# Kernel tuning notes

Hardware: AMD Instinct MI355X
Metric: run time of the kernel (lower is better)

The kernel has to match this reference:

```python
import jax, jax.numpy as jnp
import numpy as np

B, S = 4096, 256
D = 32  # output_size // 4


def setup_inputs() -> dict:
    key = jax.random.key(0)
    ks = jax.random.split(key, 32)
    # continuous features
    cont_p = jax.random.normal(ks[0], (B, S, 3), dtype=jnp.float32)
    cont_c = jax.random.normal(ks[1], (B, S, 2), dtype=jnp.float32)
    # categorical features, per-column vocab sizes from Embedding tables
    vocabs_p = [2, 2, 2, 11, 34]
    cat_p = jnp.stack([
        jax.random.randint(ks[2 + i], (B, S), 0, v, dtype=jnp.int32)
        for i, v in enumerate(vocabs_p)], axis=2)
    vocabs_c = [19, 31]
    cat_c = jnp.stack([
        jax.random.randint(ks[7 + i], (B, S), 0, v, dtype=jnp.int32)
        for i, v in enumerate(vocabs_c)], axis=2)
    lengths = jax.random.randint(ks[9], (B,), 1, S + 1, dtype=jnp.int32)

    def lin(k, fan_in, fan_out):
        bound = 1.0 / np.sqrt(fan_in)
        kw, kb = jax.random.split(k)
        w = jax.random.uniform(kw, (fan_in, fan_out), jnp.float32, -bound, bound)
        b = jax.random.uniform(kb, (fan_out,), jnp.float32, -bound, bound)
        return w, b

    w_p1, b_p1 = lin(ks[10], 3, D)
    w_p2, b_p2 = lin(ks[11], D, D)
    w_c1, b_c1 = lin(ks[12], 2, D)
    w_c2, b_c2 = lin(ks[13], D, D)
    emb_gender = jax.random.normal(ks[14], (2, D), dtype=jnp.float32)
    emb_korean = jax.random.normal(ks[15], (2, D), dtype=jnp.float32)
    emb_primary = jax.random.normal(ks[16], (2, D), dtype=jnp.float32)
    emb_job = jax.random.normal(ks[17], (11, D), dtype=jnp.float32)
    emb_rep = jax.random.normal(ks[18], (34, D), dtype=jnp.float32)
    emb_place = jax.random.normal(ks[19], (19, D), dtype=jnp.float32)
    emb_add = jax.random.normal(ks[20], (31, D), dtype=jnp.float32)
    w_fc1, b_fc1 = lin(ks[21], 128, 64)
    w_fc2, b_fc2 = lin(ks[22], 64, 2)

    return dict(cont_p=cont_p, cont_c=cont_c, cat_p=cat_p, cat_c=cat_c,
                lengths=lengths,
                w_p1=w_p1, b_p1=b_p1, w_p2=w_p2, b_p2=b_p2,
                w_c1=w_c1, b_c1=b_c1, w_c2=w_c2, b_c2=b_c2,
                emb_gender=emb_gender, emb_korean=emb_korean,
                emb_primary=emb_primary, emb_job=emb_job, emb_rep=emb_rep,
                emb_place=emb_place, emb_add=emb_add,
                w_fc1=w_fc1, b_fc1=b_fc1, w_fc2=w_fc2, b_fc2=b_fc2)


def reference(cont_p, cont_c, cat_p, cat_c, lengths,
              w_p1, b_p1, w_p2, b_p2, w_c1, b_c1, w_c2, b_c2,
              emb_gender, emb_korean, emb_primary, emb_job, emb_rep,
              emb_place, emb_add, w_fc1, b_fc1, w_fc2, b_fc2):
    # small per-token MLPs on continuous features -> [B,S,D]
    hp = jax.nn.relu(cont_p @ w_p1 + b_p1) @ w_p2 + b_p2
    hc = jax.nn.relu(cont_c @ w_c1 + b_c1) @ w_c2 + b_c2
    # multi-table embedding lookups, averaged per group -> [B,S,D]
    ep = (emb_gender[cat_p[:, :, 0]] + emb_korean[cat_p[:, :, 1]] +
          emb_primary[cat_p[:, :, 2]] + emb_job[cat_p[:, :, 3]] +
          emb_rep[cat_p[:, :, 4]]) / 5.0
    ec = (emb_place[cat_c[:, :, 0]] + emb_add[cat_c[:, :, 1]]) / 2.0
    # concat order matches torch: (cat_p, cat_c, cont_p, cont_c) -> [B,S,128]
    x = jnp.concatenate([ep, ec, hp, hc], axis=2)
    # ragged mean pool over first lengths[i] positions (masked segment mean)
    mask = (jnp.arange(x.shape[1])[None, :] < lengths[:, None])
    pooled = jnp.sum(x * mask[:, :, None], axis=1) / lengths[:, None].astype(x.dtype)
    # head: relu(fc1) -> relu(fc2); dropout p=0.0 is identity
    h = jax.nn.relu(pooled @ w_fc1 + b_fc1)
    return jax.nn.relu(h @ w_fc2 + b_fc2)
```

## Files before the change

kernel.cpp:

```cpp
#include <hip/hip_runtime.h>


#define BDIM 64

__global__ __launch_bounds__(BDIM)
void mlpreg_kernel(const float* __restrict__ cont_p,
                   const float* __restrict__ cont_c,
                   const int* __restrict__ cat_p,
                   const int* __restrict__ cat_c,
                   const int* __restrict__ lengths,
                   const float* __restrict__ w_p1, const float* __restrict__ b_p1,
                   const float* __restrict__ w_p2, const float* __restrict__ b_p2,
                   const float* __restrict__ w_c1, const float* __restrict__ b_c1,
                   const float* __restrict__ w_c2, const float* __restrict__ b_c2,
                   const float* __restrict__ emb_g,  const float* __restrict__ emb_k,
                   const float* __restrict__ emb_pr, const float* __restrict__ emb_j,
                   const float* __restrict__ emb_r,  const float* __restrict__ emb_pl,
                   const float* __restrict__ emb_a,
                   const float* __restrict__ w_fc1, const float* __restrict__ b_fc1,
                   const float* __restrict__ w_fc2, const float* __restrict__ b_fc2,
                   float* __restrict__ out)
{
    constexpr int S = 256;
    __shared__ float sP[2][S * 3];
    __shared__ float sC[2][S * 2];
    __shared__ int   hist[2][96];
    __shared__ float sPacc[2][64];
    __shared__ float sPool[2][128];

    const int lane = threadIdx.x;
    const int b0 = blockIdx.x * 2, b1 = b0 + 1;

    int L0 = lengths[b0]; L0 = (L0 < 1) ? 1 : (L0 > S ? S : L0);
    int L1 = lengths[b1]; L1 = (L1 < 1) ? 1 : (L1 > S ? S : L1);
    const float L0f = (float)L0, L1f = (float)L1;
    const float invL0 = 1.0f / L0f, invL1 = 1.0f / L1f;

    { int i = lane;            ((int*)hist)[i] = 0;
      i += 64;                 ((int*)hist)[i] = 0;
      i += 64;                 ((int*)hist)[i] = 0; }

    const int ch = lane & 31, h = lane >> 5;
    const float wp0 = w_p1[ch], wp1 = w_p1[32 + ch], wp2 = w_p1[64 + ch], bp = b_p1[ch];
    const float wc0 = w_c1[ch], wc1 = w_c1[32 + ch], bc = b_c1[ch];

    {
        const float4* gp0 = (const float4*)(cont_p + (size_t)b0 * (S * 3));
        const float4* gp1 = (const float4*)(cont_p + (size_t)b1 * (S * 3));
        const float4* gc0 = (const float4*)(cont_c + (size_t)b0 * (S * 2));
        const float4* gc1 = (const float4*)(cont_c + (size_t)b1 * (S * 2));
        const int n0 = (3 * L0 + 3) >> 2, n1 = (3 * L1 + 3) >> 2;
        const int m0 = (2 * L0 + 3) >> 2, m1 = (2 * L1 + 3) >> 2;
        for (int i = lane; i < n0; i += 64) *(float4*)&sP[0][4 * i] = gp0[i];
        for (int i = lane; i < n1; i += 64) *(float4*)&sP[1][4 * i] = gp1[i];
        for (int i = lane; i < m0; i += 64) *(float4*)&sC[0][4 * i] = gc0[i];
        for (int i = lane; i < m1; i += 64) *(float4*)&sC[1][4 * i] = gc1[i];
    }

    int sg0 = 0, sk0 = 0, sp0 = 0, sg1 = 0, sk1 = 0, sp1 = 0;
    {
        const int*  kp0 = cat_p + (size_t)b0 * (S * 5);
        const int*  kp1 = cat_p + (size_t)b1 * (S * 5);
        const int2* kc0 = (const int2*)(cat_c + (size_t)b0 * (S * 2));
        const int2* kc1 = (const int2*)(cat_c + (size_t)b1 * (S * 2));
        #pragma unroll 2
        for (int t = lane; t < L0; t += 64) {
            int v0 = kp0[5 * t], v1 = kp0[5 * t + 1], v2 = kp0[5 * t + 2],
                v3 = kp0[5 * t + 3], v4 = kp0[5 * t + 4];
            int2 q = kc0[t];
            sg0 += v0; sk0 += v1; sp0 += v2;
            atomicAdd(&hist[0][v3], 1);
            atomicAdd(&hist[0][11 + v4], 1);
            atomicAdd(&hist[0][45 + q.x], 1);
            atomicAdd(&hist[0][64 + q.y], 1);
        }
        #pragma unroll 2
        for (int t = lane; t < L1; t += 64) {
            int v0 = kp1[5 * t], v1 = kp1[5 * t + 1], v2 = kp1[5 * t + 2],
                v3 = kp1[5 * t + 3], v4 = kp1[5 * t + 4];
            int2 q = kc1[t];
            sg1 += v0; sk1 += v1; sp1 += v2;
            atomicAdd(&hist[1][v3], 1);
            atomicAdd(&hist[1][11 + v4], 1);
            atomicAdd(&hist[1][45 + q.x], 1);
            atomicAdd(&hist[1][64 + q.y], 1);
        }
    }
    #pragma unroll
    for (int d = 32; d; d >>= 1) {
        sg0 += __shfl_xor(sg0, d); sk0 += __shfl_xor(sk0, d); sp0 += __shfl_xor(sp0, d);
        sg1 += __shfl_xor(sg1, d); sk1 += __shfl_xor(sk1, d); sp1 += __shfl_xor(sp1, d);
    }
    __syncthreads();

    {
        const int   Lr   = h ? L1 : L0;
        const float invr = h ? invL1 : invL0;
        const float* tp = sP[h];
        const float* tc = sC[h];
        float aP = 0.f, aC = 0.f;
        #pragma unroll 4
        for (int t = 0; t < Lr; ++t) {
            float c0 = tp[3 * t], c1 = tp[3 * t + 1], c2 = tp[3 * t + 2];
            float2 d2 = *(const float2*)&tc[2 * t];
            aP += fmaxf(fmaf(c0, wp0, fmaf(c1, wp1, fmaf(c2, wp2, bp))), 0.f);
            aC += fmaxf(fmaf(d2.x, wc0, fmaf(d2.y, wc1, bc)), 0.f);
        }
        sPacc[h][ch]      = aP * invr;
        sPacc[h][32 + ch] = aC * invr;
    }
    __syncthreads();

    if (h == 0) {
        float g0 = emb_g[ch],  g1 = emb_g[32 + ch];
        float k0 = emb_k[ch],  k1 = emb_k[32 + ch];
        float p0 = emb_pr[ch], p1 = emb_pr[32 + ch];
        float fg0 = (float)sg0, fk0 = (float)sk0, fp0 = (float)sp0;
        float fg1 = (float)sg1, fk1 = (float)sk1, fp1 = (float)sp1;
        float A0 = fmaf(L0f - fg0, g0, fg0 * g1) + fmaf(L0f - fk0, k0, fk0 * k1)
                 + fmaf(L0f - fp0, p0, fp0 * p1);
        float A1 = fmaf(L1f - fg1, g0, fg1 * g1) + fmaf(L1f - fk1, k0, fk1 * k1)
                 + fmaf(L1f - fp1, p0, fp1 * p1);
        #pragma unroll
        for (int r = 0; r < 11; ++r) {
            float w = emb_j[r * 32 + ch];
            A0 = fmaf((float)hist[0][r], w, A0);
            A1 = fmaf((float)hist[1][r], w, A1);
        }
        #pragma unroll
        for (int r = 0; r < 34; ++r) {
            float w = emb_r[r * 32 + ch];
            A0 = fmaf((float)hist[0][11 + r], w, A0);
            A1 = fmaf((float)hist[1][11 + r], w, A1);
        }
        sPool[0][ch] = A0 * (invL0 * 0.2f);
        sPool[1][ch] = A1 * (invL1 * 0.2f);

        float v0 = b_p2[ch], v1 = v0;
        #pragma unroll
        for (int k = 0; k < 32; ++k) {
            float w = w_p2[k * 32 + ch];
            v0 = fmaf(sPacc[0][k], w, v0);
            v1 = fmaf(sPacc[1][k], w, v1);
        }
        sPool[0][64 + ch] = v0;
        sPool[1][64 + ch] = v1;
    } else {
        float A0 = 0.f, A1 = 0.f;
        #pragma unroll
        for (int r = 0; r < 19; ++r) {
            float w = emb_pl[r * 32 + ch];
            A0 = fmaf((float)hist[0][45 + r], w, A0);
            A1 = fmaf((float)hist[1][45 + r], w, A1);
        }
        #pragma unroll
        for (int r = 0; r < 31; ++r) {
            float w = emb_a[r * 32 + ch];
            A0 = fmaf((float)hist[0][64 + r], w, A0);
            A1 = fmaf((float)hist[1][64 + r], w, A1);
        }
        sPool[0][32 + ch] = A0 * (invL0 * 0.5f);
        sPool[1][32 + ch] = A1 * (invL1 * 0.5f);

        float v0 = b_c2[ch], v1 = v0;
        #pragma unroll
        for (int k = 0; k < 32; ++k) {
            float w = w_c2[k * 32 + ch];
            v0 = fmaf(sPacc[0][32 + k], w, v0);
            v1 = fmaf(sPacc[1][32 + k], w, v1);
        }
        sPool[0][96 + ch] = v0;
        sPool[1][96 + ch] = v1;
    }
    __syncthreads();

    {
        const int o = lane;
        float x0 = b_fc1[o], y0 = 0.f;
        float x1 = x0,       y1 = 0.f;
        #pragma unroll 8
        for (int k = 0; k < 128; k += 2) {
            float wa = w_fc1[(size_t)k * 64 + o];
            float wb = w_fc1[(size_t)(k + 1) * 64 + o];
            float u0 = sPool[0][k], u1 = sPool[0][k + 1];
            float s0 = sPool[1][k], s1 = sPool[1][k + 1];
            x0 = fmaf(u0, wa, x0); y0 = fmaf(u1, wb, y0);
            x1 = fmaf(s0, wa, x1); y1 = fmaf(s1, wb, y1);
        }
        float h0 = fmaxf(x0 + y0, 0.f);
        float h1 = fmaxf(x1 + y1, 0.f);
        float wa = w_fc2[2 * o], wb = w_fc2[2 * o + 1];
        float q00 = h0 * wa, q01 = h0 * wb, q10 = h1 * wa, q11 = h1 * wb;
        #pragma unroll
        for (int d = 32; d; d >>= 1) {
            q00 += __shfl_xor(q00, d); q01 += __shfl_xor(q01, d);
            q10 += __shfl_xor(q10, d); q11 += __shfl_xor(q11, d);
        }
        if (lane == 0) {
            float bb0 = b_fc2[0], bb1 = b_fc2[1];
            float4 o4;
            o4.x = fmaxf(q00 + bb0, 0.f);
            o4.y = fmaxf(q01 + bb1, 0.f);
            o4.z = fmaxf(q10 + bb0, 0.f);
            o4.w = fmaxf(q11 + bb1, 0.f);
            *(float4*)&out[(size_t)b0 * 2] = o4;
        }
    }
}

extern "C" void kernel_launch(void* const* d_in, const int* in_sizes, int n_in,
                              void* d_out, int out_size, void* d_ws, size_t ws_size,
                              hipStream_t stream) {
    const float* cont_p = (const float*)d_in[0];
    const float* cont_c = (const float*)d_in[1];
    const int*   cat_p  = (const int*)d_in[2];
    const int*   cat_c  = (const int*)d_in[3];
    const int*   lens   = (const int*)d_in[4];
    const float* w_p1   = (const float*)d_in[5];
    const float* b_p1   = (const float*)d_in[6];
    const float* w_p2   = (const float*)d_in[7];
    const float* b_p2   = (const float*)d_in[8];
    const float* w_c1   = (const float*)d_in[9];
    const float* b_c1   = (const float*)d_in[10];
    const float* w_c2   = (const float*)d_in[11];
    const float* b_c2   = (const float*)d_in[12];
    const float* emb_g  = (const float*)d_in[13];
    const float* emb_k  = (const float*)d_in[14];
    const float* emb_pr = (const float*)d_in[15];
    const float* emb_j  = (const float*)d_in[16];
    const float* emb_r  = (const float*)d_in[17];
    const float* emb_pl = (const float*)d_in[18];
    const float* emb_a  = (const float*)d_in[19];
    const float* w_fc1  = (const float*)d_in[20];
    const float* b_fc1  = (const float*)d_in[21];
    const float* w_fc2  = (const float*)d_in[22];
    const float* b_fc2  = (const float*)d_in[23];
    float* out = (float*)d_out;

    hipLaunchKernelGGL(mlpreg_kernel, dim3(2048), dim3(BDIM), 0, stream,
                       cont_p, cont_c, cat_p, cat_c, lens,
                       w_p1, b_p1, w_p2, b_p2, w_c1, b_c1, w_c2, b_c2,
                       emb_g, emb_k, emb_pr, emb_j, emb_r, emb_pl, emb_a,
                       w_fc1, b_fc1, w_fc2, b_fc2, out);
}
```

Baseline: 139.9 us.

## Interleave token features in shared memory, pack categorical sums, vectorize fc1

Continuous features for each token are now staged into one interleaved shared array with a stride of 8, so the per-token MLP loop reads a float4 plus a scalar instead of five scattered loads. The three binary categorical sums are packed into a single int with 10-bit fields, cutting the warp shuffle reductions from six values to two. The histogram loop is unrolled into four fixed 64-token blocks, and the fc1 loop reads pooled vectors as float4. The staging loop now does scalar loads with a divide by 3 instead of float4 copies, which adds integer work and non-vector global loads.

```diff
diff --git a/kernel.cpp b/kernel.cpp
--- a/kernel.cpp
+++ b/kernel.cpp
@@ -2,6 +2,7 @@
 
 
 #define BDIM 64
+#define S 256
 
 __global__ __launch_bounds__(BDIM)
 void mlpreg_kernel(const float* __restrict__ cont_p,
@@ -21,93 +22,92 @@
                    const float* __restrict__ w_fc2, const float* __restrict__ b_fc2,
                    float* __restrict__ out)
 {
-    constexpr int S = 256;
-    __shared__ float sP[2][S * 3];
-    __shared__ float sC[2][S * 2];
+    __shared__ __align__(16) float sTok[2][S * 8];
     __shared__ int   hist[2][96];
     __shared__ float sPacc[2][64];
-    __shared__ float sPool[2][128];
+    __shared__ __align__(16) float sPool[2][128];
 
     const int lane = threadIdx.x;
     const int b0 = blockIdx.x * 2, b1 = b0 + 1;
-
-    int L0 = lengths[b0]; L0 = (L0 < 1) ? 1 : (L0 > S ? S : L0);
-    int L1 = lengths[b1]; L1 = (L1 < 1) ? 1 : (L1 > S ? S : L1);
+    int2 ll = *(const int2*)&lengths[b0];
+    int L0 = ll.x; L0 = (L0 < 1) ? 1 : (L0 > S ? S : L0);
+    int L1 = ll.y; L1 = (L1 < 1) ? 1 : (L1 > S ? S : L1);
     const float L0f = (float)L0, L1f = (float)L1;
     const float invL0 = 1.0f / L0f, invL1 = 1.0f / L1f;
 
-    { int i = lane;            ((int*)hist)[i] = 0;
-      i += 64;                 ((int*)hist)[i] = 0;
-      i += 64;                 ((int*)hist)[i] = 0; }
+    ((int*)hist)[lane]       = 0;
+    ((int*)hist)[64 + lane]  = 0;
+    ((int*)hist)[128 + lane] = 0;
 
     const int ch = lane & 31, h = lane >> 5;
     const float wp0 = w_p1[ch], wp1 = w_p1[32 + ch], wp2 = w_p1[64 + ch], bp = b_p1[ch];
     const float wc0 = w_c1[ch], wc1 = w_c1[32 + ch], bc = b_c1[ch];
 
-    {
-        const float4* gp0 = (const float4*)(cont_p + (size_t)b0 * (S * 3));
-        const float4* gp1 = (const float4*)(cont_p + (size_t)b1 * (S * 3));
-        const float4* gc0 = (const float4*)(cont_c + (size_t)b0 * (S * 2));
-        const float4* gc1 = (const float4*)(cont_c + (size_t)b1 * (S * 2));
-        const int n0 = (3 * L0 + 3) >> 2, n1 = (3 * L1 + 3) >> 2;
-        const int m0 = (2 * L0 + 3) >> 2, m1 = (2 * L1 + 3) >> 2;
-        for (int i = lane; i < n0; i += 64) *(float4*)&sP[0][4 * i] = gp0[i];
-        for (int i = lane; i < n1; i += 64) *(float4*)&sP[1][4 * i] = gp1[i];
-        for (int i = lane; i < m0; i += 64) *(float4*)&sC[0][4 * i] = gc0[i];
-        for (int i = lane; i < m1; i += 64) *(float4*)&sC[1][4 * i] = gc1[i];
-    }
-
-    int sg0 = 0, sk0 = 0, sp0 = 0, sg1 = 0, sk1 = 0, sp1 = 0;
-    {
-        const int*  kp0 = cat_p + (size_t)b0 * (S * 5);
-        const int*  kp1 = cat_p + (size_t)b1 * (S * 5);
-        const int2* kc0 = (const int2*)(cat_c + (size_t)b0 * (S * 2));
-        const int2* kc1 = (const int2*)(cat_c + (size_t)b1 * (S * 2));
-        #pragma unroll 2
-        for (int t = lane; t < L0; t += 64) {
-            int v0 = kp0[5 * t], v1 = kp0[5 * t + 1], v2 = kp0[5 * t + 2],
-                v3 = kp0[5 * t + 3], v4 = kp0[5 * t + 4];
-            int2 q = kc0[t];
-            sg0 += v0; sk0 += v1; sp0 += v2;
-            atomicAdd(&hist[0][v3], 1);
-            atomicAdd(&hist[0][11 + v4], 1);
-            atomicAdd(&hist[0][45 + q.x], 1);
-            atomicAdd(&hist[0][64 + q.y], 1);
-        }
-        #pragma unroll 2
-        for (int t = lane; t < L1; t += 64) {
-            int v0 = kp1[5 * t], v1 = kp1[5 * t + 1], v2 = kp1[5 * t + 2],
-                v3 = kp1[5 * t + 3], v4 = kp1[5 * t + 4];
-            int2 q = kc1[t];
-            sg1 += v0; sk1 += v1; sp1 += v2;
-            atomicAdd(&hist[1][v3], 1);
-            atomicAdd(&hist[1][11 + v4], 1);
-            atomicAdd(&hist[1][45 + q.x], 1);
-            atomicAdd(&hist[1][64 + q.y], 1);
+    const float* gp[2] = { cont_p + (size_t)b0 * (S * 3), cont_p + (size_t)b1 * (S * 3) };
+    const float* gc[2] = { cont_c + (size_t)b0 * (S * 2), cont_c + (size_t)b1 * (S * 2) };
+    const int*   kp[2] = { cat_p  + (size_t)b0 * (S * 5), cat_p  + (size_t)b1 * (S * 5) };
+    const int*   kc[2] = { cat_c  + (size_t)b0 * (S * 2), cat_c  + (size_t)b1 * (S * 2) };
+    const int    Ls[2] = { L0, L1 };
+
+    #pragma unroll
+    for (int r = 0; r < 2; ++r) {
+        const int n3 = 3 * Ls[r], n2 = 2 * Ls[r];
+        for (int i = lane; i < n3; i += BDIM) {
+            int t = i / 3, c = i - 3 * t;
+            sTok[r][t * 8 + c] = gp[r][i];
+        }
+        for (int i = lane; i < n2; i += BDIM) {
+            int t = i >> 1, c = i & 1;
+            sTok[r][t * 8 + 3 + c] = gc[r][i];
+        }
+    }
+
+    int pk0 = 0, pk1 = 0;
+    #pragma unroll
+    for (int r = 0; r < 2; ++r) {
+        #pragma unroll
+        for (int blk = 0; blk < 4; ++blk) {
+            if (Ls[r] > blk * 64) {
+                int t = blk * 64 + lane;
+                if (t < Ls[r]) {
+                    int v0 = kp[r][5 * t], v1 = kp[r][5 * t + 1], v2 = kp[r][5 * t + 2],
+                        v3 = kp[r][5 * t + 3], v4 = kp[r][5 * t + 4];
+                    int2 q = *(const int2*)&kc[r][2 * t];
+                    int add = v0 + (v1 << 10) + (v2 << 20);
+                    if (r == 0) pk0 += add; else pk1 += add;
+                    atomicAdd(&hist[r][v3], 1);
+                    atomicAdd(&hist[r][11 + v4], 1);
+                    atomicAdd(&hist[r][45 + q.x], 1);
+                    atomicAdd(&hist[r][64 + q.y], 1);
+                }
+            }
         }
     }
     #pragma unroll
     for (int d = 32; d; d >>= 1) {
-        sg0 += __shfl_xor(sg0, d); sk0 += __shfl_xor(sk0, d); sp0 += __shfl_xor(sp0, d);
-        sg1 += __shfl_xor(sg1, d); sk1 += __shfl_xor(sk1, d); sp1 += __shfl_xor(sp1, d);
-    }
+        pk0 += __shfl_xor(pk0, d);
+        pk1 += __shfl_xor(pk1, d);
+    }
+    const float sg0 = (float)(pk0 & 1023), sk0 = (float)((pk0 >> 10) & 1023),
+                sp0 = (float)(pk0 >> 20);
+    const float sg1 = (float)(pk1 & 1023), sk1 = (float)((pk1 >> 10) & 1023),
+                sp1 = (float)(pk1 >> 20);
     __syncthreads();
 
     {
-        const int   Lr   = h ? L1 : L0;
-        const float invr = h ? invL1 : invL0;
-        const float* tp = sP[h];
-        const float* tc = sC[h];
-        float aP = 0.f, aC = 0.f;
-        #pragma unroll 4
-        for (int t = 0; t < Lr; ++t) {
-            float c0 = tp[3 * t], c1 = tp[3 * t + 1], c2 = tp[3 * t + 2];
-            float2 d2 = *(const float2*)&tc[2 * t];
-            aP += fmaxf(fmaf(c0, wp0, fmaf(c1, wp1, fmaf(c2, wp2, bp))), 0.f);
-            aC += fmaxf(fmaf(d2.x, wc0, fmaf(d2.y, wc1, bc)), 0.f);
-        }
-        sPacc[h][ch]      = aP * invr;
-        sPacc[h][32 + ch] = aC * invr;
+        const float* tok  = sTok[h];
+        const int    myL  = h ? L1 : L0;
+        const float  invr = h ? invL1 : invL0;
+        float accP = 0.f, accC = 0.f;
+        #pragma unroll 2
+        for (int t = 0; t < myL; ++t) {
+            float4 v  = *(const float4*)&tok[t * 8];
+            float  c1 = tok[t * 8 + 4];
+            accP += fmaxf(fmaf(v.x, wp0, fmaf(v.y, wp1, fmaf(v.z, wp2, bp))), 0.f);
+            accC += fmaxf(fmaf(v.w, wc0, fmaf(c1, wc1, bc)), 0.f);
+        }
+        sPacc[h][ch]      = accP * invr;
+        sPacc[h][32 + ch] = accC * invr;
     }
     __syncthreads();
 
@@ -115,12 +115,10 @@
         float g0 = emb_g[ch],  g1 = emb_g[32 + ch];
         float k0 = emb_k[ch],  k1 = emb_k[32 + ch];
         float p0 = emb_pr[ch], p1 = emb_pr[32 + ch];
-        float fg0 = (float)sg0, fk0 = (float)sk0, fp0 = (float)sp0;
-        float fg1 = (float)sg1, fk1 = (float)sk1, fp1 = (float)sp1;
-        float A0 = fmaf(L0f - fg0, g0, fg0 * g1) + fmaf(L0f - fk0, k0, fk0 * k1)
-                 + fmaf(L0f - fp0, p0, fp0 * p1);
-        float A1 = fmaf(L1f - fg1, g0, fg1 * g1) + fmaf(L1f - fk1, k0, fk1 * k1)
-                 + fmaf(L1f - fp1, p0, fp1 * p1);
+        float A0 = fmaf(L0f - sg0, g0, sg0 * g1) + fmaf(L0f - sk0, k0, sk0 * k1)
+                 + fmaf(L0f - sp0, p0, sp0 * p1);
+        float A1 = fmaf(L1f - sg1, g0, sg1 * g1) + fmaf(L1f - sk1, k0, sk1 * k1)
+                 + fmaf(L1f - sp1, p0, sp1 * p1);
         #pragma unroll
         for (int r = 0; r < 11; ++r) {
             float w = emb_j[r * 32 + ch];
@@ -178,17 +176,22 @@
         const int o = lane;
         float x0 = b_fc1[o], y0 = 0.f;
         float x1 = x0,       y1 = 0.f;
-        #pragma unroll 8
-        for (int k = 0; k < 128; k += 2) {
-            float wa = w_fc1[(size_t)k * 64 + o];
-            float wb = w_fc1[(size_t)(k + 1) * 64 + o];
-            float u0 = sPool[0][k], u1 = sPool[0][k + 1];
-            float s0 = sPool[1][k], s1 = sPool[1][k + 1];
-            x0 = fmaf(u0, wa, x0); y0 = fmaf(u1, wb, y0);
-            x1 = fmaf(s0, wa, x1); y1 = fmaf(s1, wb, y1);
+        #pragma unroll
+        for (int k4 = 0; k4 < 32; ++k4) {
+            float4 u = *(const float4*)&sPool[0][4 * k4];
+            float4 s = *(const float4*)&sPool[1][4 * k4];
+            float wa = w_fc1[(size_t)(4 * k4 + 0) * 64 + o];
+            float wb = w_fc1[(size_t)(4 * k4 + 1) * 64 + o];
+            float wc = w_fc1[(size_t)(4 * k4 + 2) * 64 + o];
+            float wd = w_fc1[(size_t)(4 * k4 + 3) * 64 + o];
+            x0 = fmaf(u.x, wa, x0); y0 = fmaf(u.y, wb, y0);
+            x0 = fmaf(u.z, wc, x0); y0 = fmaf(u.w, wd, y0);
+            x1 = fmaf(s.x, wa, x1); y1 = fmaf(s.y, wb, y1);
+            x1 = fmaf(s.z, wc, x1); y1 = fmaf(s.w, wd, y1);
         }
         float h0 = fmaxf(x0 + y0, 0.f);
         float h1 = fmaxf(x1 + y1, 0.f);
+
         float wa = w_fc2[2 * o], wb = w_fc2[2 * o + 1];
         float q00 = h0 * wa, q01 = h0 * wb, q10 = h1 * wa, q11 = h1 * wb;
         #pragma unroll
```

Result: slower. 150.1 us (+7.3%).
